# Optimization experiments

Measured on AMD Instinct MI355X. Metric: run time of the kernel, lower is better.

The kernel has to match this reference:

```python
import jax, jax.numpy as jnp
import numpy as np

N_NODES = 100000


def gcn_conv(x, src, dst, W, b, n_nodes):
    # x: [N, Fin], src/dst: [E'] (self-loops already included)
    h = x @ W  # [N, Fout] transform first (Fout <= Fin friendly)
    ones = jnp.ones(src.shape[0], dtype=x.dtype)
    deg = jax.ops.segment_sum(ones, dst, num_segments=n_nodes)  # in-degree with self-loops
    dinv = jnp.where(deg > 0, jax.lax.rsqrt(deg), 0.0)
    norm = dinv[src] * dinv[dst]  # [E']
    msg = h[src] * norm[:, None]  # gather + scale
    out = jax.ops.segment_sum(msg, dst, num_segments=n_nodes)  # scatter-add
    return out + b


def setup_inputs() -> dict:
    key = jax.random.key(0)
    ks = jax.random.split(key, 5)
    n, e, fin, hid, ncls = N_NODES, 3200000, 128, 64, 11
    x = jax.random.normal(ks[0], (n, fin), dtype=jnp.float32)
    edge_index = jax.random.randint(ks[1], (2, e), 0, n, dtype=jnp.int64)
    W1 = jax.random.normal(ks[2], (fin, hid), dtype=jnp.float32) * (1.0 / np.sqrt(fin))
    b1 = jnp.zeros((hid,), dtype=jnp.float32)
    W2 = jax.random.normal(ks[3], (hid, hid), dtype=jnp.float32) * (1.0 / np.sqrt(hid))
    b2 = jnp.zeros((hid,), dtype=jnp.float32)
    Wfc = jax.random.normal(ks[4], (hid, ncls), dtype=jnp.float32) * (1.0 / np.sqrt(hid))
    bfc = jnp.zeros((ncls,), dtype=jnp.float32)
    return {"x": x, "edge_index": edge_index, "W1": W1, "b1": b1,
            "W2": W2, "b2": b2, "Wfc": Wfc, "bfc": bfc}


def reference(x, edge_index, W1, b1, W2, b2, Wfc, bfc):
    n = x.shape[0]
    loops = jnp.arange(n, dtype=edge_index.dtype)
    src = jnp.concatenate([edge_index[0], loops])  # add self-loops (GCNConv default)
    dst = jnp.concatenate([edge_index[1], loops])
    h = gcn_conv(x, src, dst, W1, b1, n)
    h = jax.nn.relu(h)  # dropout is identity in eval mode
    h = gcn_conv(h, src, dst, W2, b2, n)
    h = jax.nn.relu(h)
    return h @ Wfc + bfc
```

## Files before the change

### kernel.cpp

```cpp
#include <hip/hip_runtime.h>
#include <hip/hip_fp16.h>

#define HID 64
#define SH 9
#define BKN 512
#define MAXB1 256
#define NBLK 512
typedef unsigned int u32;

__global__ __launch_bounds__(256) void count_chunks(const int* __restrict__ dst,
                                                    int* __restrict__ cnt2,
                                                    int E, int nbk) {
  __shared__ int lc[MAXB1];
  const int t = threadIdx.x;
  for (int b = t; b < nbk; b += 256) lc[b] = 0;
  __syncthreads();
  const int C = (E + NBLK - 1) / NBLK;
  const int s0 = blockIdx.x * C;
  const int s1 = min(s0 + C, E);
  for (int i = s0 + t; i < s1; i += 256) atomicAdd(&lc[dst[i] >> SH], 1);
  __syncthreads();
  for (int b = t; b < nbk; b += 256)
    cnt2[(size_t)b * NBLK + blockIdx.x] = lc[b];
}

__global__ __launch_bounds__(256) void scan_blocks(const int* __restrict__ v_in,
                                                   int* __restrict__ excl,
                                                   int* __restrict__ bsum, int n) {
  __shared__ int s[256];
  const int t = threadIdx.x;
  const int i = blockIdx.x * 256 + t;
  const int v = (i < n) ? v_in[i] : 0;
  s[t] = v;
  __syncthreads();
  for (int off = 1; off < 256; off <<= 1) {
    const int u = (t >= off) ? s[t - off] : 0;
    __syncthreads();
    s[t] += u;
    __syncthreads();
  }
  if (i < n) excl[i] = s[t] - v;
  if (t == 255) bsum[blockIdx.x] = s[255];
}

__global__ __launch_bounds__(512) void scan_top(int* bsum, int nb) {
  __shared__ int s[512];
  const int t = threadIdx.x;
  const int v = (t < nb) ? bsum[t] : 0;
  s[t] = v;
  __syncthreads();
  for (int off = 1; off < 512; off <<= 1) {
    const int u = (t >= off) ? s[t - off] : 0;
    __syncthreads();
    s[t] += u;
    __syncthreads();
  }
  if (t < nb) bsum[t] = s[t] - v;
}

__global__ __launch_bounds__(256) void add_offsets2(int* __restrict__ off,
                                                    const int* __restrict__ bsum,
                                                    int* __restrict__ boff,
                                                    int NE, int E, int nbk) {
  const int m = blockIdx.x * 256 + threadIdx.x;
  if (m < NE) {
    const int v = off[m] + bsum[blockIdx.x];
    off[m] = v;
    if ((m & (NBLK - 1)) == 0) boff[m >> 9] = v;
  }
  if (m == 0) boff[nbk] = E;
}

__global__ __launch_bounds__(512) void fill_pairs(const int* __restrict__ src,
                                                  const int* __restrict__ dst,
                                                  const int* __restrict__ off,
                                                  u32* __restrict__ pairs,
                                                  int E, int nbk) {
  __shared__ int lbase[MAXB1];
  __shared__ int lrank[MAXB1];
  const int t = threadIdx.x;
  for (int b = t; b < nbk; b += 512) {
    lbase[b] = off[(size_t)b * NBLK + blockIdx.x];
    lrank[b] = 0;
  }
  __syncthreads();
  const int C = (E + NBLK - 1) / NBLK;
  const int s0 = blockIdx.x * C;
  const int s1 = min(s0 + C, E);
  for (int i = s0 + t; i < s1; i += 512) {
    const int d = dst[i];
    const int b = d >> SH;
    const int r = atomicAdd(&lrank[b], 1);
    pairs[lbase[b] + r] = ((u32)(d & (BKN - 1)) << 17) | (u32)src[i];
  }
}

__global__ __launch_bounds__(1024) void bucket_csr(const u32* __restrict__ pairs,
                                                   const int* __restrict__ boff,
                                                   int* __restrict__ rowptr,
                                                   int* __restrict__ rowend,
                                                   float* __restrict__ dinv,
                                                   int* __restrict__ colidx,
                                                   int n, int nbk) {
  __shared__ int ldeg[BKN];
  __shared__ int lofs[BKN];
  const int bkt = blockIdx.x;
  const int t = threadIdx.x;
  if (t < BKN) ldeg[t] = 0;
  __syncthreads();
  const int beg = boff[bkt], end = boff[bkt + 1];
  const int cnt = end - beg;
  for (int e = t; e < cnt; e += 1024)
    atomicAdd(&ldeg[pairs[beg + e] >> 17], 1);
  __syncthreads();
  const int node = bkt * BKN + t;
  int dg = 0, pdg = 0;
  if (t < BKN) {
    dg = ldeg[t];
    pdg = (node < n) ? ((dg + 1 + 7) & ~7) : 0;
    lofs[t] = pdg;
  }
  __syncthreads();
  for (int o = 1; o < BKN; o <<= 1) {
    int u = 0;
    if (t < BKN && t >= o) u = lofs[t - o];
    __syncthreads();
    if (t < BKN) lofs[t] += u;
    __syncthreads();
  }
  const int pbase = beg + bkt * (BKN * 8);
  if (t < BKN && node < n) {
    const int base = pbase + lofs[t] - pdg;
    rowptr[node] = base;
    rowend[node] = base + pdg;
    dinv[node] = rsqrtf((float)(dg + 1));
    colidx[base] = node;
    for (int j = 1 + dg; j < pdg; ++j) colidx[base + j] = n;
    ldeg[t] = base + 1;
  }
  __syncthreads();
  for (int e = t; e < cnt; e += 1024) {
    const u32 p = pairs[beg + e];
    const int pos = atomicAdd(&ldeg[p >> 17], 1);
    colidx[pos] = (int)(p & 0x1FFFF);
  }
}

template <int K>
__global__ __launch_bounds__(256) void gemm_nodes(const float* __restrict__ x,
                                                  const float* __restrict__ W,
                                                  const float* __restrict__ dinv,
                                                  __half* __restrict__ out) {
  __shared__ float Wl[K * 64];
  __shared__ float xl[16][K + 4];
  const int tid = threadIdx.x;
  for (int i = tid; i < K * 16; i += 256)
    reinterpret_cast<float4*>(Wl)[i] = reinterpret_cast<const float4*>(W)[i];
  const int row0 = blockIdx.x * 16;
  for (int i = tid; i < 16 * (K / 4); i += 256) {
    const int r = i / (K / 4), q = i % (K / 4);
    reinterpret_cast<float4*>(&xl[r][0])[q] =
        reinterpret_cast<const float4*>(x + (size_t)(row0 + r) * K)[q];
  }
  __syncthreads();
  const int r = tid >> 4;
  const int cg = (tid & 15) << 2;
  float4 acc = {0.f, 0.f, 0.f, 0.f};
#pragma unroll
  for (int k = 0; k < K; k += 4) {
    const float4 xv = *reinterpret_cast<const float4*>(&xl[r][k]);
    const float4 w0 = *reinterpret_cast<const float4*>(&Wl[(k + 0) * 64 + cg]);
    const float4 w1 = *reinterpret_cast<const float4*>(&Wl[(k + 1) * 64 + cg]);
    const float4 w2 = *reinterpret_cast<const float4*>(&Wl[(k + 2) * 64 + cg]);
    const float4 w3 = *reinterpret_cast<const float4*>(&Wl[(k + 3) * 64 + cg]);
    acc.x = fmaf(xv.w, w3.x, fmaf(xv.z, w2.x, fmaf(xv.y, w1.x, fmaf(xv.x, w0.x, acc.x))));
    acc.y = fmaf(xv.w, w3.y, fmaf(xv.z, w2.y, fmaf(xv.y, w1.y, fmaf(xv.x, w0.y, acc.y))));
    acc.z = fmaf(xv.w, w3.z, fmaf(xv.z, w2.z, fmaf(xv.y, w1.z, fmaf(xv.x, w0.z, acc.z))));
    acc.w = fmaf(xv.w, w3.w, fmaf(xv.z, w2.w, fmaf(xv.y, w1.w, fmaf(xv.x, w0.w, acc.w))));
  }
  const int grow = row0 + r;
  const float di = dinv[grow];
  __half2* op = reinterpret_cast<__half2*>(out + (size_t)grow * 64 + cg);
  op[0] = __floats2half2_rn(acc.x * di, acc.y * di);
  op[1] = __floats2half2_rn(acc.z * di, acc.w * di);
}

__global__ __launch_bounds__(256) void gemm_nodes_h(const __half* __restrict__ x,
                                                    const float* __restrict__ W,
                                                    const float* __restrict__ dinv,
                                                    __half* __restrict__ out) {
  __shared__ float Wl[64 * 64];
  __shared__ float xl[16][68];
  const int tid = threadIdx.x;
  for (int i = tid; i < 64 * 16; i += 256)
    reinterpret_cast<float4*>(Wl)[i] = reinterpret_cast<const float4*>(W)[i];
  const int row0 = blockIdx.x * 16;
  if (tid < 128) {
    const int r = tid >> 3, q = tid & 7;
    const float4 hv = *reinterpret_cast<const float4*>(
        x + (size_t)(row0 + r) * 64 + q * 8);
    const __half2* hp = reinterpret_cast<const __half2*>(&hv);
#pragma unroll
    for (int j = 0; j < 4; ++j) {
      const float2 f = __half22float2(hp[j]);
      xl[r][q * 8 + 2 * j + 0] = f.x;
      xl[r][q * 8 + 2 * j + 1] = f.y;
    }
  }
  __syncthreads();
  const int r = tid >> 4;
  const int cg = (tid & 15) << 2;
  float4 acc = {0.f, 0.f, 0.f, 0.f};
#pragma unroll
  for (int k = 0; k < 64; k += 4) {
    const float4 xv = *reinterpret_cast<const float4*>(&xl[r][k]);
    const float4 w0 = *reinterpret_cast<const float4*>(&Wl[(k + 0) * 64 + cg]);
    const float4 w1 = *reinterpret_cast<const float4*>(&Wl[(k + 1) * 64 + cg]);
    const float4 w2 = *reinterpret_cast<const float4*>(&Wl[(k + 2) * 64 + cg]);
    const float4 w3 = *reinterpret_cast<const float4*>(&Wl[(k + 3) * 64 + cg]);
    acc.x = fmaf(xv.w, w3.x, fmaf(xv.z, w2.x, fmaf(xv.y, w1.x, fmaf(xv.x, w0.x, acc.x))));
    acc.y = fmaf(xv.w, w3.y, fmaf(xv.z, w2.y, fmaf(xv.y, w1.y, fmaf(xv.x, w0.y, acc.y))));
    acc.z = fmaf(xv.w, w3.z, fmaf(xv.z, w2.z, fmaf(xv.y, w1.z, fmaf(xv.x, w0.z, acc.z))));
    acc.w = fmaf(xv.w, w3.w, fmaf(xv.z, w2.w, fmaf(xv.y, w1.w, fmaf(xv.x, w0.w, acc.w))));
  }
  const int grow = row0 + r;
  const float di = dinv[grow];
  __half2* op = reinterpret_cast<__half2*>(out + (size_t)grow * 64 + cg);
  op[0] = __floats2half2_rn(acc.x * di, acc.y * di);
  op[1] = __floats2half2_rn(acc.z * di, acc.w * di);
}

__global__ __launch_bounds__(256) void gather_agg(const int* __restrict__ rowptr,
                                                  const int* __restrict__ rowend,
                                                  const int* __restrict__ colidx,
                                                  const __half2* __restrict__ g2,
                                                  const float* __restrict__ dinv,
                                                  const float* __restrict__ bias,
                                                  __half2* __restrict__ outp, int n) {
  const int lane = threadIdx.x & 63;
  const int node = (blockIdx.x * 256 + threadIdx.x) >> 6;
  if (node >= n) return;
  const int h = lane >> 5;
  const int l = lane & 31;
  const int beg = rowptr[node];
  const int end = rowend[node];
  float2 acc = {0.f, 0.f};
  int e = beg + h;
  for (; e + 30 < end; e += 32) {
    int s[16];
#pragma unroll
    for (int j = 0; j < 16; ++j) s[j] = colidx[e + 2 * j];
    float2 v[16];
#pragma unroll
    for (int j = 0; j < 16; ++j)
      v[j] = __half22float2(g2[((u32)s[j] << 5) + (u32)l]);
#pragma unroll
    for (int j = 0; j < 16; ++j) {
      acc.x += v[j].x;
      acc.y += v[j].y;
    }
  }
  for (; e + 6 < end; e += 8) {
    const int s0 = colidx[e + 0], s1 = colidx[e + 2];
    const int s2 = colidx[e + 4], s3 = colidx[e + 6];
    const float2 v0 = __half22float2(g2[((u32)s0 << 5) + (u32)l]);
    const float2 v1 = __half22float2(g2[((u32)s1 << 5) + (u32)l]);
    const float2 v2 = __half22float2(g2[((u32)s2 << 5) + (u32)l]);
    const float2 v3 = __half22float2(g2[((u32)s3 << 5) + (u32)l]);
    acc.x += (v0.x + v1.x) + (v2.x + v3.x);
    acc.y += (v0.y + v1.y) + (v2.y + v3.y);
  }
  acc.x += __shfl_xor(acc.x, 32);
  acc.y += __shfl_xor(acc.y, 32);
  const float di = dinv[node];
  const float2 bb = reinterpret_cast<const float2*>(bias)[l];
  const float rx = fmaxf(fmaf(acc.x, di, bb.x), 0.f);
  const float ry = fmaxf(fmaf(acc.y, di, bb.y), 0.f);
  if (h == 0) outp[(size_t)node * 32 + l] = __floats2half2_rn(rx, ry);
}

__global__ __launch_bounds__(256) void gemm_fc(const __half* __restrict__ h,
                                               const float* __restrict__ W,
                                               const float* __restrict__ b,
                                               float* __restrict__ out, int n) {
  __shared__ float Wl[772];
  __shared__ float xl[16][68];
  const int tid = threadIdx.x;
  for (int i = tid; i < 772; i += 256) Wl[i] = 0.f;
  __syncthreads();
  for (int i = tid; i < 64 * 11; i += 256) Wl[(i / 11) * 12 + (i % 11)] = W[i];
  const int row00 = blockIdx.x * 64;
  for (int rr = 0; rr < 4; ++rr) {
    const int row0 = row00 + rr * 16;
    __syncthreads();
    if (tid < 128) {
      const int r = tid >> 3, q = tid & 7;
      const int grow = row0 + r;
      if (grow < n) {
        const float4 hv = *reinterpret_cast<const float4*>(
            h + (size_t)grow * 64 + q * 8);
        const __half2* hp = reinterpret_cast<const __half2*>(&hv);
#pragma unroll
        for (int j = 0; j < 4; ++j) {
          const float2 f = __half22float2(hp[j]);
          xl[r][q * 8 + 2 * j + 0] = f.x;
          xl[r][q * 8 + 2 * j + 1] = f.y;
        }
      }
    }
    __syncthreads();
    const int r = tid >> 4, c = tid & 15;
    float acc = 0.f;
#pragma unroll
    for (int k = 0; k < 64; k += 4) {
      acc = fmaf(xl[r][k + 0], Wl[(k + 0) * 12 + c], acc);
      acc = fmaf(xl[r][k + 1], Wl[(k + 1) * 12 + c], acc);
      acc = fmaf(xl[r][k + 2], Wl[(k + 2) * 12 + c], acc);
      acc = fmaf(xl[r][k + 3], Wl[(k + 3) * 12 + c], acc);
    }
    const int grow = row0 + r;
    if (c < 11 && grow < n) out[(size_t)grow * 11 + c] = acc + b[c];
  }
}

extern "C" void kernel_launch(void* const* d_in, const int* in_sizes, int n_in,
                              void* d_out, int out_size, void* d_ws, size_t ws_size,
                              hipStream_t stream) {
  const float* x   = (const float*)d_in[0];
  const int*   ei  = (const int*)d_in[1];
  const float* W1  = (const float*)d_in[2];
  const float* b1  = (const float*)d_in[3];
  const float* W2  = (const float*)d_in[4];
  const float* b2  = (const float*)d_in[5];
  const float* Wfc = (const float*)d_in[6];
  const float* bfc = (const float*)d_in[7];
  float* out = (float*)d_out;

  const int n = in_sizes[0] / 128;
  const int E = in_sizes[1] / 2;
  const int* src = ei;
  const int* dst = ei + E;
  const int nbk = (n + BKN - 1) >> SH;
  const int NE = nbk * NBLK;

  char* ws = (char*)d_ws;
  size_t o = 0;
  auto alloc = [&](size_t bytes) {
    char* p = ws + o;
    o += (bytes + 255) & ~(size_t)255;
    return p;
  };
  float*  dinv   = (float*) alloc((size_t)n * 4);
  int*    rowptr = (int*)   alloc((size_t)n * 4);
  int*    rowend = (int*)   alloc((size_t)n * 4);
  int*    cnt2   = (int*)   alloc((size_t)NE * 4);
  int*    off    = (int*)   alloc((size_t)NE * 4);
  int*    bsum2  = (int*)   alloc(512 * 4);
  int*    boff   = (int*)   alloc((size_t)(nbk + 1) * 4);
  u32*    pairs  = (u32*)   alloc((size_t)E * 4);
  int*    colidx = (int*)   alloc(((size_t)E + (size_t)nbk * BKN * 8) * 4);
  __half* B0h    = (__half*)alloc((size_t)(n + 1) * HID * 2);
  __half* B1h    = (__half*)alloc((size_t)n * HID * 2);
  if (o > ws_size) return;

  const int nb2 = (NE + 255) / 256;
  const int gblocks = n / 16;
  const int fcblocks = (n + 63) / 64;

  hipMemsetAsync(B0h + (size_t)n * HID, 0, HID * 2, stream);

  count_chunks<<<NBLK, 256, 0, stream>>>(dst, cnt2, E, nbk);
  scan_blocks<<<nb2, 256, 0, stream>>>(cnt2, off, bsum2, NE);
  scan_top<<<1, 512, 0, stream>>>(bsum2, nb2);
  add_offsets2<<<nb2, 256, 0, stream>>>(off, bsum2, boff, NE, E, nbk);
  fill_pairs<<<NBLK, 512, 0, stream>>>(src, dst, off, pairs, E, nbk);
  bucket_csr<<<nbk, 1024, 0, stream>>>(pairs, boff, rowptr, rowend, dinv,
                                       colidx, n, nbk);

  const int pull_blocks = (n * 64 + 255) / 256;

  gemm_nodes<128><<<gblocks, 256, 0, stream>>>(x, W1, dinv, B0h);
  gather_agg<<<pull_blocks, 256, 0, stream>>>(rowptr, rowend, colidx,
      (const __half2*)B0h, dinv, b1, (__half2*)B1h, n);

  gemm_nodes_h<<<gblocks, 256, 0, stream>>>(B1h, W2, dinv, B0h);
  gather_agg<<<pull_blocks, 256, 0, stream>>>(rowptr, rowend, colidx,
      (const __half2*)B0h, dinv, b2, (__half2*)B1h, n);

  gemm_fc<<<fcblocks, 256, 0, stream>>>(B1h, Wfc, bfc, out, n);
}
```

Before: 251.2 us.

## Use MFMA f16 matrix instructions for both node-transform GEMMs

Replaces the scalar FMA GEMM kernels for both layers with MFMA 16x16x32 f16 kernels that process 64 rows per block. x and W are converted to fp16 in LDS, and W is stored transposed. This removes the per-thread FMA loops and reduces block count. The trade-offs are fp16 rounding of inputs and weights, scalar 2-byte output stores, and redundant weight conversion in every block. The GEMMs are likely a small share of total time next to the CSR build and gather.

```diff
diff --git a/kernel.cpp b/kernel.cpp
--- a/kernel.cpp
+++ b/kernel.cpp
@@ -7,6 +7,9 @@
 #define MAXB1 256
 #define NBLK 512
 typedef unsigned int u32;
+typedef float f32x4 __attribute__((ext_vector_type(4)));
+typedef _Float16 f16x4 __attribute__((ext_vector_type(4)));
+typedef _Float16 f16x8 __attribute__((ext_vector_type(8)));
 
 __global__ __launch_bounds__(256) void count_chunks(const int* __restrict__ dst,
                                                     int* __restrict__ cnt2,
@@ -146,88 +149,137 @@
   }
 }
 
-template <int K>
-__global__ __launch_bounds__(256) void gemm_nodes(const float* __restrict__ x,
+__global__ __launch_bounds__(256) void gemm1_mfma(const float* __restrict__ x,
                                                   const float* __restrict__ W,
                                                   const float* __restrict__ dinv,
-                                                  __half* __restrict__ out) {
-  __shared__ float Wl[K * 64];
-  __shared__ float xl[16][K + 4];
+                                                  __half* __restrict__ out, int n) {
+  __shared__ _Float16 Ah[64 * 136];
+  __shared__ _Float16 Wt[64 * 136];
   const int tid = threadIdx.x;
-  for (int i = tid; i < K * 16; i += 256)
-    reinterpret_cast<float4*>(Wl)[i] = reinterpret_cast<const float4*>(W)[i];
-  const int row0 = blockIdx.x * 16;
-  for (int i = tid; i < 16 * (K / 4); i += 256) {
-    const int r = i / (K / 4), q = i % (K / 4);
-    reinterpret_cast<float4*>(&xl[r][0])[q] =
-        reinterpret_cast<const float4*>(x + (size_t)(row0 + r) * K)[q];
-  }
-  __syncthreads();
-  const int r = tid >> 4;
-  const int cg = (tid & 15) << 2;
-  float4 acc = {0.f, 0.f, 0.f, 0.f};
-#pragma unroll
-  for (int k = 0; k < K; k += 4) {
-    const float4 xv = *reinterpret_cast<const float4*>(&xl[r][k]);
-    const float4 w0 = *reinterpret_cast<const float4*>(&Wl[(k + 0) * 64 + cg]);
-    const float4 w1 = *reinterpret_cast<const float4*>(&Wl[(k + 1) * 64 + cg]);
-    const float4 w2 = *reinterpret_cast<const float4*>(&Wl[(k + 2) * 64 + cg]);
-    const float4 w3 = *reinterpret_cast<const float4*>(&Wl[(k + 3) * 64 + cg]);
-    acc.x = fmaf(xv.w, w3.x, fmaf(xv.z, w2.x, fmaf(xv.y, w1.x, fmaf(xv.x, w0.x, acc.x))));
-    acc.y = fmaf(xv.w, w3.y, fmaf(xv.z, w2.y, fmaf(xv.y, w1.y, fmaf(xv.x, w0.y, acc.y))));
-    acc.z = fmaf(xv.w, w3.z, fmaf(xv.z, w2.z, fmaf(xv.y, w1.z, fmaf(xv.x, w0.z, acc.z))));
-    acc.w = fmaf(xv.w, w3.w, fmaf(xv.z, w2.w, fmaf(xv.y, w1.w, fmaf(xv.x, w0.w, acc.w))));
-  }
-  const int grow = row0 + r;
-  const float di = dinv[grow];
-  __half2* op = reinterpret_cast<__half2*>(out + (size_t)grow * 64 + cg);
-  op[0] = __floats2half2_rn(acc.x * di, acc.y * di);
-  op[1] = __floats2half2_rn(acc.z * di, acc.w * di);
-}
-
-__global__ __launch_bounds__(256) void gemm_nodes_h(const __half* __restrict__ x,
-                                                    const float* __restrict__ W,
-                                                    const float* __restrict__ dinv,
-                                                    __half* __restrict__ out) {
-  __shared__ float Wl[64 * 64];
-  __shared__ float xl[16][68];
+  const int row0 = blockIdx.x * 64;
+  for (int i = tid; i < 64 * 32; i += 256) {
+    const int r = i >> 5, q = i & 31;
+    const int gr = row0 + r;
+    float4 v = {0.f, 0.f, 0.f, 0.f};
+    if (gr < n) v = reinterpret_cast<const float4*>(x)[(size_t)gr * 32 + q];
+    f16x4 hv = {(_Float16)v.x, (_Float16)v.y, (_Float16)v.z, (_Float16)v.w};
+    *reinterpret_cast<f16x4*>(&Ah[r * 136 + q * 4]) = hv;
+  }
+  for (int i = tid; i < 64 * 32; i += 256) {
+    const int c = i & 63, k0 = (i >> 6) * 4;
+    f16x4 hv = {(_Float16)W[(size_t)(k0 + 0) * 64 + c],
+                (_Float16)W[(size_t)(k0 + 1) * 64 + c],
+                (_Float16)W[(size_t)(k0 + 2) * 64 + c],
+                (_Float16)W[(size_t)(k0 + 3) * 64 + c]};
+    *reinterpret_cast<f16x4*>(&Wt[c * 136 + k0]) = hv;
+  }
+  __syncthreads();
+  const int lane = tid & 63;
+  const int m = lane & 15, g = lane >> 4;
+  const int r0 = (tid >> 6) * 16;
+  f32x4 acc0 = {0.f, 0.f, 0.f, 0.f}, acc1 = acc0, acc2 = acc0, acc3 = acc0;
+  const _Float16* arow = &Ah[(r0 + m) * 136];
+#pragma unroll
+  for (int kc = 0; kc < 4; ++kc) {
+    const int ko = kc * 32 + g * 4;
+    const f16x4 alo = *reinterpret_cast<const f16x4*>(arow + ko);
+    const f16x4 ahi = *reinterpret_cast<const f16x4*>(arow + ko + 16);
+    const f16x8 a = __builtin_shufflevector(alo, ahi, 0, 1, 2, 3, 4, 5, 6, 7);
+    const f16x4 bl0 = *reinterpret_cast<const f16x4*>(&Wt[(0  + m) * 136 + ko]);
+    const f16x4 bh0 = *reinterpret_cast<const f16x4*>(&Wt[(0  + m) * 136 + ko + 16]);
+    const f16x4 bl1 = *reinterpret_cast<const f16x4*>(&Wt[(16 + m) * 136 + ko]);
+    const f16x4 bh1 = *reinterpret_cast<const f16x4*>(&Wt[(16 + m) * 136 + ko + 16]);
+    const f16x4 bl2 = *reinterpret_cast<const f16x4*>(&Wt[(32 + m) * 136 + ko]);
+    const f16x4 bh2 = *reinterpret_cast<const f16x4*>(&Wt[(32 + m) * 136 + ko + 16]);
+    const f16x4 bl3 = *reinterpret_cast<const f16x4*>(&Wt[(48 + m) * 136 + ko]);
+    const f16x4 bh3 = *reinterpret_cast<const f16x4*>(&Wt[(48 + m) * 136 + ko + 16]);
+    const f16x8 b0 = __builtin_shufflevector(bl0, bh0, 0, 1, 2, 3, 4, 5, 6, 7);
+    const f16x8 b1 = __builtin_shufflevector(bl1, bh1, 0, 1, 2, 3, 4, 5, 6, 7);
+    const f16x8 b2 = __builtin_shufflevector(bl2, bh2, 0, 1, 2, 3, 4, 5, 6, 7);
+    const f16x8 b3 = __builtin_shufflevector(bl3, bh3, 0, 1, 2, 3, 4, 5, 6, 7);
+    acc0 = __builtin_amdgcn_mfma_f32_16x16x32_f16(a, b0, acc0, 0, 0, 0);
+    acc1 = __builtin_amdgcn_mfma_f32_16x16x32_f16(a, b1, acc1, 0, 0, 0);
+    acc2 = __builtin_amdgcn_mfma_f32_16x16x32_f16(a, b2, acc2, 0, 0, 0);
+    acc3 = __builtin_amdgcn_mfma_f32_16x16x32_f16(a, b3, acc3, 0, 0, 0);
+  }
+  _Float16* o16 = reinterpret_cast<_Float16*>(out);
+#pragma unroll
+  for (int j = 0; j < 4; ++j) {
+    const int grow = row0 + r0 + g * 4 + j;
+    if (grow < n) {
+      const float di = dinv[grow];
+      o16[(size_t)grow * 64 + 0  + m] = (_Float16)(acc0[j] * di);
+      o16[(size_t)grow * 64 + 16 + m] = (_Float16)(acc1[j] * di);
+      o16[(size_t)grow * 64 + 32 + m] = (_Float16)(acc2[j] * di);
+      o16[(size_t)grow * 64 + 48 + m] = (_Float16)(acc3[j] * di);
+    }
+  }
+}
+
+__global__ __launch_bounds__(256) void gemm2_mfma(const __half* __restrict__ h,
+                                                  const float* __restrict__ W,
+                                                  const float* __restrict__ dinv,
+                                                  __half* __restrict__ out, int n) {
+  __shared__ _Float16 Ah[64 * 72];
+  __shared__ _Float16 Wt[64 * 72];
   const int tid = threadIdx.x;
-  for (int i = tid; i < 64 * 16; i += 256)
-    reinterpret_cast<float4*>(Wl)[i] = reinterpret_cast<const float4*>(W)[i];
-  const int row0 = blockIdx.x * 16;
-  if (tid < 128) {
-    const int r = tid >> 3, q = tid & 7;
-    const float4 hv = *reinterpret_cast<const float4*>(
-        x + (size_t)(row0 + r) * 64 + q * 8);
-    const __half2* hp = reinterpret_cast<const __half2*>(&hv);
-#pragma unroll
-    for (int j = 0; j < 4; ++j) {
-      const float2 f = __half22float2(hp[j]);
-      xl[r][q * 8 + 2 * j + 0] = f.x;
-      xl[r][q * 8 + 2 * j + 1] = f.y;
+  const int row0 = blockIdx.x * 64;
+  for (int i = tid; i < 64 * 8; i += 256) {
+    const int r = i >> 3, q = i & 7;
+    const int gr = row0 + r;
+    float4 raw = {0.f, 0.f, 0.f, 0.f};
+    if (gr < n) raw = reinterpret_cast<const float4*>(h)[(size_t)gr * 8 + q];
+    *reinterpret_cast<float4*>(&Ah[r * 72 + q * 8]) = raw;
+  }
+  for (int i = tid; i < 64 * 16; i += 256) {
+    const int c = i & 63, k0 = (i >> 6) * 4;
+    f16x4 hv = {(_Float16)W[(size_t)(k0 + 0) * 64 + c],
+                (_Float16)W[(size_t)(k0 + 1) * 64 + c],
+                (_Float16)W[(size_t)(k0 + 2) * 64 + c],
+                (_Float16)W[(size_t)(k0 + 3) * 64 + c]};
+    *reinterpret_cast<f16x4*>(&Wt[c * 72 + k0]) = hv;
+  }
+  __syncthreads();
+  const int lane = tid & 63;
+  const int m = lane & 15, g = lane >> 4;
+  const int r0 = (tid >> 6) * 16;
+  f32x4 acc0 = {0.f, 0.f, 0.f, 0.f}, acc1 = acc0, acc2 = acc0, acc3 = acc0;
+  const _Float16* arow = &Ah[(r0 + m) * 72];
+#pragma unroll
+  for (int kc = 0; kc < 2; ++kc) {
+    const int ko = kc * 32 + g * 4;
+    const f16x4 alo = *reinterpret_cast<const f16x4*>(arow + ko);
+    const f16x4 ahi = *reinterpret_cast<const f16x4*>(arow + ko + 16);
+    const f16x8 a = __builtin_shufflevector(alo, ahi, 0, 1, 2, 3, 4, 5, 6, 7);
+    const f16x4 bl0 = *reinterpret_cast<const f16x4*>(&Wt[(0  + m) * 72 + ko]);
+    const f16x4 bh0 = *reinterpret_cast<const f16x4*>(&Wt[(0  + m) * 72 + ko + 16]);
+    const f16x4 bl1 = *reinterpret_cast<const f16x4*>(&Wt[(16 + m) * 72 + ko]);
+    const f16x4 bh1 = *reinterpret_cast<const f16x4*>(&Wt[(16 + m) * 72 + ko + 16]);
+    const f16x4 bl2 = *reinterpret_cast<const f16x4*>(&Wt[(32 + m) * 72 + ko]);
+    const f16x4 bh2 = *reinterpret_cast<const f16x4*>(&Wt[(32 + m) * 72 + ko + 16]);
+    const f16x4 bl3 = *reinterpret_cast<const f16x4*>(&Wt[(48 + m) * 72 + ko]);
+    const f16x4 bh3 = *reinterpret_cast<const f16x4*>(&Wt[(48 + m) * 72 + ko + 16]);
+    const f16x8 b0 = __builtin_shufflevector(bl0, bh0, 0, 1, 2, 3, 4, 5, 6, 7);
+    const f16x8 b1 = __builtin_shufflevector(bl1, bh1, 0, 1, 2, 3, 4, 5, 6, 7);
+    const f16x8 b2 = __builtin_shufflevector(bl2, bh2, 0, 1, 2, 3, 4, 5, 6, 7);
+    const f16x8 b3 = __builtin_shufflevector(bl3, bh3, 0, 1, 2, 3, 4, 5, 6, 7);
+    acc0 = __builtin_amdgcn_mfma_f32_16x16x32_f16(a, b0, acc0, 0, 0, 0);
+    acc1 = __builtin_amdgcn_mfma_f32_16x16x32_f16(a, b1, acc1, 0, 0, 0);
+    acc2 = __builtin_amdgcn_mfma_f32_16x16x32_f16(a, b2, acc2, 0, 0, 0);
+    acc3 = __builtin_amdgcn_mfma_f32_16x16x32_f16(a, b3, acc3, 0, 0, 0);
+  }
+  _Float16* o16 = reinterpret_cast<_Float16*>(out);
+#pragma unroll
+  for (int j = 0; j < 4; ++j) {
+    const int grow = row0 + r0 + g * 4 + j;
+    if (grow < n) {
+      const float di = dinv[grow];
+      o16[(size_t)grow * 64 + 0  + m] = (_Float16)(acc0[j] * di);
+      o16[(size_t)grow * 64 + 16 + m] = (_Float16)(acc1[j] * di);
+      o16[(size_t)grow * 64 + 32 + m] = (_Float16)(acc2[j] * di);
+      o16[(size_t)grow * 64 + 48 + m] = (_Float16)(acc3[j] * di);
     }
   }
-  __syncthreads();
-  const int r = tid >> 4;
-  const int cg = (tid & 15) << 2;
-  float4 acc = {0.f, 0.f, 0.f, 0.f};
-#pragma unroll
-  for (int k = 0; k < 64; k += 4) {
-    const float4 xv = *reinterpret_cast<const float4*>(&xl[r][k]);
-    const float4 w0 = *reinterpret_cast<const float4*>(&Wl[(k + 0) * 64 + cg]);
-    const float4 w1 = *reinterpret_cast<const float4*>(&Wl[(k + 1) * 64 + cg]);
-    const float4 w2 = *reinterpret_cast<const float4*>(&Wl[(k + 2) * 64 + cg]);
-    const float4 w3 = *reinterpret_cast<const float4*>(&Wl[(k + 3) * 64 + cg]);
-    acc.x = fmaf(xv.w, w3.x, fmaf(xv.z, w2.x, fmaf(xv.y, w1.x, fmaf(xv.x, w0.x, acc.x))));
-    acc.y = fmaf(xv.w, w3.y, fmaf(xv.z, w2.y, fmaf(xv.y, w1.y, fmaf(xv.x, w0.y, acc.y))));
-    acc.z = fmaf(xv.w, w3.z, fmaf(xv.z, w2.z, fmaf(xv.y, w1.z, fmaf(xv.x, w0.z, acc.z))));
-    acc.w = fmaf(xv.w, w3.w, fmaf(xv.z, w2.w, fmaf(xv.y, w1.w, fmaf(xv.x, w0.w, acc.w))));
-  }
-  const int grow = row0 + r;
-  const float di = dinv[grow];
-  __half2* op = reinterpret_cast<__half2*>(out + (size_t)grow * 64 + cg);
-  op[0] = __floats2half2_rn(acc.x * di, acc.y * di);
-  op[1] = __floats2half2_rn(acc.z * di, acc.w * di);
 }
 
 __global__ __launch_bounds__(256) void gather_agg(const int* __restrict__ rowptr,
@@ -364,7 +416,7 @@
   if (o > ws_size) return;
 
   const int nb2 = (NE + 255) / 256;
-  const int gblocks = n / 16;
+  const int gblocks = (n + 63) / 64;
   const int fcblocks = (n + 63) / 64;
 
   hipMemsetAsync(B0h + (size_t)n * HID, 0, HID * 2, stream);
@@ -379,11 +431,11 @@
 
   const int pull_blocks = (n * 64 + 255) / 256;
 
-  gemm_nodes<128><<<gblocks, 256, 0, stream>>>(x, W1, dinv, B0h);
+  gemm1_mfma<<<gblocks, 256, 0, stream>>>(x, W1, dinv, B0h, n);
   gather_agg<<<pull_blocks, 256, 0, stream>>>(rowptr, rowend, colidx,
       (const __half2*)B0h, dinv, b1, (__half2*)B1h, n);
 
-  gemm_nodes_h<<<gblocks, 256, 0, stream>>>(B1h, W2, dinv, B0h);
+  gemm2_mfma<<<gblocks, 256, 0, stream>>>(B1h, W2, dinv, B0h, n);
   gather_agg<<<pull_blocks, 256, 0, stream>>>(rowptr, rowend, colidx,
       (const __half2*)B0h, dinv, b2, (__half2*)B1h, n);
 
```

Measured after the change: 219.3 us. 1.15x faster.
